# Performance work log

Measured on AMD Instinct MI355X. Metric: run time of the kernel, lower is better.

## Reference

```python
import jax, jax.numpy as jnp
import numpy as np

D_MODEL = 1024
NUM_HEADS = 16
HEAD_DIM = D_MODEL // NUM_HEADS


def setup_inputs() -> dict:
    key = jax.random.key(0)
    ks = jax.random.split(key, 9)
    B, S = 4, 2048
    bound = 1.0 / np.sqrt(D_MODEL)  # nn.Linear default init range
    def lin(kw, kb):
        W = jax.random.uniform(kw, (D_MODEL, D_MODEL), jnp.float32, -bound, bound)
        b = jax.random.uniform(kb, (D_MODEL,), jnp.float32, -bound, bound)
        return W, b
    Wq, bq = lin(ks[0], ks[1])
    Wk, bk = lin(ks[2], ks[3])
    Wv, bv = lin(ks[4], ks[5])
    Wo, bo = lin(ks[6], ks[7])
    x = jax.random.normal(ks[8], (B, S, D_MODEL), jnp.float32)
    return {"x": x, "Wq": Wq, "bq": bq, "Wk": Wk, "bk": bk,
            "Wv": Wv, "bv": bv, "Wo": Wo, "bo": bo}


def reference(x, Wq, bq, Wk, bk, Wv, bv, Wo, bo):
    B, S, _ = x.shape
    scale = 1.0 / np.sqrt(HEAD_DIM)
    # projections; torch Linear is x @ W.T + b; here W stored as [in, out]-style [d,d] already transposed
    def split_heads(t):
        return t.reshape(B, S, NUM_HEADS, HEAD_DIM).transpose(0, 2, 1, 3)  # [B,H,S,Dh]
    q = split_heads(x @ Wq + bq)
    k = split_heads(x @ Wk + bk)
    v = split_heads(x @ Wv + bv)
    scores = jnp.einsum('bhqd,bhkd->bhqk', q, k) * scale  # [B,H,S,S]
    attn = jax.nn.softmax(scores, axis=-1)
    out = jnp.einsum('bhqk,bhkd->bhqd', attn, v)  # [B,H,S,Dh]
    out = out.transpose(0, 2, 1, 3).reshape(B, S, D_MODEL)
    return out @ Wo + bo
```

## Files before the change

kernel.cpp:

```cpp
#include <hip/hip_runtime.h>
#include <hip/hip_bf16.h>

typedef __attribute__((ext_vector_type(8))) short short8;
typedef __attribute__((ext_vector_type(4))) float f32x4;
typedef __attribute__((ext_vector_type(16))) float f32x16;

#define MFMA16(a, b, c) __builtin_amdgcn_mfma_f32_16x16x32_bf16((a), (b), (c), 0, 0, 0)
#define MFMA32(a, b, c) __builtin_amdgcn_mfma_f32_32x32x16_bf16((a), (b), (c), 0, 0, 0)

__device__ __forceinline__ void gload_lds16(const void* g, void* l) {
  __builtin_amdgcn_global_load_lds(
      (const __attribute__((address_space(1))) unsigned int*)g,
      (__attribute__((address_space(3))) unsigned int*)l, 16, 0, 0);
}

__global__ __launch_bounds__(256) void cvt_x(const float* __restrict__ x,
                                             __hip_bfloat16* __restrict__ xb) {
  size_t i = ((size_t)blockIdx.x * 256 + threadIdx.x) * 8;
  float4 a = *(const float4*)(x + i);
  float4 b = *(const float4*)(x + i + 4);
  struct alignas(16) B8 { __hip_bfloat16 h[8]; } o;
  o.h[0] = __float2bfloat16(a.x); o.h[1] = __float2bfloat16(a.y);
  o.h[2] = __float2bfloat16(a.z); o.h[3] = __float2bfloat16(a.w);
  o.h[4] = __float2bfloat16(b.x); o.h[5] = __float2bfloat16(b.y);
  o.h[6] = __float2bfloat16(b.z); o.h[7] = __float2bfloat16(b.w);
  *(B8*)(xb + i) = o;
}

__global__ __launch_bounds__(256) void trans_w(const float* __restrict__ W0,
                                               const float* __restrict__ W1,
                                               const float* __restrict__ W2,
                                               const float* __restrict__ W3,
                                               __hip_bfloat16* __restrict__ Wt) {
  const int which = blockIdx.z;
  const float* W = (which == 0) ? W0 : (which == 1) ? W1 : (which == 2) ? W2 : W3;
  __hip_bfloat16* O = Wt + (size_t)which * 1024 * 1024;
  __shared__ __hip_bfloat16 lds[64][65];
  const int k0 = blockIdx.y * 64, n0 = blockIdx.x * 64;
#pragma unroll
  for (int i = 0; i < 16; ++i) {
    int idx = threadIdx.x + i * 256;
    int r = idx >> 6, c = idx & 63;
    lds[r][c] = __float2bfloat16(W[(size_t)(k0 + r) * 1024 + n0 + c]);
  }
  __syncthreads();
#pragma unroll
  for (int i = 0; i < 16; ++i) {
    int idx = threadIdx.x + i * 256;
    int r = idx >> 6, c = idx & 63;
    O[(size_t)(n0 + r) * 1024 + k0 + c] = lds[c][r];
  }
}

__global__ __launch_bounds__(256) void gemm_qkv(const __hip_bfloat16* __restrict__ A,
                                                const __hip_bfloat16* __restrict__ Wt,
                                                const float* __restrict__ bq,
                                                const float* __restrict__ bk,
                                                const float* __restrict__ bv,
                                                __hip_bfloat16* __restrict__ Qb,
                                                __hip_bfloat16* __restrict__ Kb,
                                                __hip_bfloat16* __restrict__ Vtb) {
  const int K = 1024;
  __shared__ __hip_bfloat16 Asm[128 * 32];
  __shared__ __hip_bfloat16 Bsm[128 * 32];
  const int t = threadIdx.x;
  const int lane = t & 63, w = t >> 6, g = lane >> 4;
  const int bid = (blockIdx.x & 7) * 192 + (blockIdx.x >> 3);
  const int mb0 = (bid / 24) * 128;
  const int nbg = (bid % 24) * 128;
  const int which = nbg >> 10;
  const int nb0 = nbg & 1023;
  const __hip_bfloat16* Bt = Wt + (size_t)which * 1048576;
  const float* bias = (which == 0) ? bq : (which == 1) ? bk : bv;
  const int wr = (w >> 1) * 64, wc = (w & 1) * 64;
  f32x4 acc[4][4] = {};

  for (int k0 = 0; k0 < K; k0 += 32) {
    __syncthreads();
#pragma unroll
    for (int i = 0; i < 2; ++i) {
      int tp = i * 256 + t;
      int row = tp >> 2;
      int slot = (tp & 3) ^ ((row >> 1) & 3);
      gload_lds16(A + (size_t)(mb0 + row) * K + k0 + slot * 8,
                  (char*)Asm + (i * 256 + w * 64) * 16);
    }
#pragma unroll
    for (int i = 0; i < 2; ++i) {
      int tp = i * 256 + t;
      int row = tp >> 2;
      int slot = (tp & 3) ^ ((row >> 1) & 3);
      gload_lds16(Bt + (size_t)(nb0 + row) * K + k0 + slot * 8,
                  (char*)Bsm + (i * 256 + w * 64) * 16);
    }
    asm volatile("s_waitcnt vmcnt(0)" ::: "memory");
    __syncthreads();

    short8 a[4], b[4];
#pragma unroll
    for (int m = 0; m < 4; ++m) {
      int row = wr + m * 16 + (lane & 15);
      a[m] = *(const short8*)((const char*)Asm + row * 64 + ((g ^ ((row >> 1) & 3)) * 16));
    }
#pragma unroll
    for (int n = 0; n < 4; ++n) {
      int row = wc + n * 16 + (lane & 15);
      b[n] = *(const short8*)((const char*)Bsm + row * 64 + ((g ^ ((row >> 1) & 3)) * 16));
    }
#pragma unroll
    for (int m = 0; m < 4; ++m)
#pragma unroll
      for (int n = 0; n < 4; ++n)
        acc[m][n] = MFMA16(a[m], b[n], acc[m][n]);
  }

#pragma unroll
  for (int n = 0; n < 4; ++n) {
    int col = nb0 + wc + n * 16 + (lane & 15);
    float bvv = bias[col];
#pragma unroll
    for (int m = 0; m < 4; ++m) {
#pragma unroll
      for (int r = 0; r < 4; ++r) {
        int row = mb0 + wr + m * 16 + g * 4 + r;
        __hip_bfloat16 hv = __float2bfloat16(acc[m][n][r] + bvv);
        if (which == 2) {
          int bb = row >> 11, s = row & 2047;
          int sp = (s & ~12) | ((s & 4) << 1) | ((s & 8) >> 1);
          Vtb[((size_t)(bb * 1024 + col) << 11) + sp] = hv;
        } else {
          __hip_bfloat16* O = which ? Kb : Qb;
          O[(size_t)row * 1024 + col] = hv;
        }
      }
    }
  }
}

__global__ __launch_bounds__(256) void gemm_o(const __hip_bfloat16* __restrict__ A,
                                              const __hip_bfloat16* __restrict__ Bt,
                                              const float* __restrict__ bias,
                                              float* __restrict__ outp) {
  const int N = 1024, K = 1024;
  __shared__ __hip_bfloat16 Asm[128 * 32];
  __shared__ __hip_bfloat16 Bsm[128 * 32];
  const int t = threadIdx.x;
  const int lane = t & 63, w = t >> 6, g = lane >> 4;
  const int bid = (blockIdx.x & 7) * 64 + (blockIdx.x >> 3);
  const int mb0 = (bid / 8) * 128;
  const int nb0 = (bid % 8) * 128;
  const int wr = (w >> 1) * 64, wc = (w & 1) * 64;
  f32x4 acc[4][4] = {};

  for (int k0 = 0; k0 < K; k0 += 32) {
    __syncthreads();
#pragma unroll
    for (int i = 0; i < 2; ++i) {
      int tp = i * 256 + t;
      int row = tp >> 2;
      int slot = (tp & 3) ^ ((row >> 1) & 3);
      gload_lds16(A + (size_t)(mb0 + row) * K + k0 + slot * 8,
                  (char*)Asm + (i * 256 + w * 64) * 16);
      gload_lds16(Bt + (size_t)(nb0 + row) * K + k0 + slot * 8,
                  (char*)Bsm + (i * 256 + w * 64) * 16);
    }
    asm volatile("s_waitcnt vmcnt(0)" ::: "memory");
    __syncthreads();

    short8 a[4], b[4];
#pragma unroll
    for (int m = 0; m < 4; ++m) {
      int row = wr + m * 16 + (lane & 15);
      a[m] = *(const short8*)((const char*)Asm + row * 64 + ((g ^ ((row >> 1) & 3)) * 16));
    }
#pragma unroll
    for (int n = 0; n < 4; ++n) {
      int row = wc + n * 16 + (lane & 15);
      b[n] = *(const short8*)((const char*)Bsm + row * 64 + ((g ^ ((row >> 1) & 3)) * 16));
    }
#pragma unroll
    for (int m = 0; m < 4; ++m)
#pragma unroll
      for (int n = 0; n < 4; ++n)
        acc[m][n] = MFMA16(a[m], b[n], acc[m][n]);
  }

#pragma unroll
  for (int n = 0; n < 4; ++n) {
    int col = nb0 + wc + n * 16 + (lane & 15);
    float bvv = bias[col];
#pragma unroll
    for (int m = 0; m < 4; ++m)
#pragma unroll
      for (int r = 0; r < 4; ++r) {
        int row = mb0 + wr + m * 16 + g * 4 + r;
        outp[(size_t)row * N + col] = acc[m][n][r] + bvv;
      }
  }
}

__global__ __launch_bounds__(256, 2) void attn_fwd8(const __hip_bfloat16* __restrict__ Q,
                                                    const __hip_bfloat16* __restrict__ Kg,
                                                    const __hip_bfloat16* __restrict__ Vt,
                                                    __hip_bfloat16* __restrict__ ctx) {
  __shared__ __hip_bfloat16 Ksm[2][64 * 64];
  __shared__ __hip_bfloat16 Vsm[2][64 * 64];
  const int t = threadIdx.x, lane = t & 63, w = t >> 6;
  const int l31 = lane & 31, hi = lane >> 5;
  const int bid = (blockIdx.x & 7) * 64 + (blockIdx.x >> 3);
  const int bh = bid >> 3, qt = bid & 7;
  const int b = bh >> 4, h = bh & 15;
  const int qA = qt * 256 + w * 64 + l31;
  const int qB = qA + 32;

  short8 qfA[4], qfB[4];
  {
    const __hip_bfloat16* qp = Q + ((size_t)(b * 2048 + qA)) * 1024 + h * 64 + hi * 8;
#pragma unroll
    for (int c = 0; c < 4; ++c) qfA[c] = *(const short8*)(qp + 16 * c);
    qp += 32 * 1024;
#pragma unroll
    for (int c = 0; c < 4; ++c) qfB[c] = *(const short8*)(qp + 16 * c);
  }
  const __hip_bfloat16* Kbh = Kg + (size_t)b * 2048 * 1024 + h * 64;
  const __hip_bfloat16* Vbh = Vt + (size_t)(b * 16 + h) * 64 * 2048;

  const int srow = t >> 3;
  const int sslot = t & 7;

#define STAGE(buf, ktn)                                                          \
  do {                                                                           \
    _Pragma("unroll") for (int i = 0; i < 2; ++i) {                              \
      int row = i * 32 + srow;                                                   \
      int sl = sslot ^ (row & 7);                                                \
      gload_lds16(Kbh + (size_t)((ktn) + row) * 1024 + sl * 8,                   \
                  (char*)&Ksm[buf][0] + i * 4096 + w * 1024);                    \
      gload_lds16(Vbh + (size_t)row * 2048 + (ktn) + sl * 8,                     \
                  (char*)&Vsm[buf][0] + i * 4096 + w * 1024);                    \
    }                                                                            \
  } while (0)

  f32x16 otA0 = {}, otA1 = {}, otB0 = {}, otB1 = {};
  float lsA0 = 0.f, lsA1 = 0.f, lsB0 = 0.f, lsB1 = 0.f;
  const float CL = 0.18033688011112042f;
  const float NEG = -43.28085122666891f;

  STAGE(0, 0);
  asm volatile("s_waitcnt vmcnt(0)" ::: "memory");
  __syncthreads();

  for (int kt = 0; kt < 2048; kt += 64) {
    const int cur = (kt >> 6) & 1;
    if (kt + 64 < 2048) STAGE(cur ^ 1, kt + 64);

    const char* Kb0 = (const char*)&Ksm[cur][0];
    const char* Vb0 = (const char*)&Vsm[cur][0];

    f32x16 sA0 = {}, sA1 = {}, sB0 = {}, sB1 = {};
    {
      short8 kf[2][4];
#pragma unroll
      for (int s = 0; s < 2; ++s)
#pragma unroll
        for (int c = 0; c < 4; ++c) {
          int row = s * 32 + l31;
          kf[s][c] = *(const short8*)(Kb0 + row * 128 + (((hi + 2 * c) ^ (row & 7)) * 16));
        }
#pragma unroll
      for (int c = 0; c < 4; ++c) {
        sA0 = MFMA32(kf[0][c], qfA[c], sA0);
        sA1 = MFMA32(kf[1][c], qfA[c], sA1);
        sB0 = MFMA32(kf[0][c], qfB[c], sB0);
        sB1 = MFMA32(kf[1][c], qfB[c], sB1);
      }
    }

    short8 vf[2][4];
#pragma unroll
    for (int dt = 0; dt < 2; ++dt)
#pragma unroll
      for (int c = 0; c < 4; ++c) {
        int row = dt * 32 + l31;
        vf[dt][c] = *(const short8*)(Vb0 + row * 128 + (((hi + 2 * c) ^ (row & 7)) * 16));
      }

    {
      unsigned ua[16];
#pragma unroll
      for (int n = 0; n < 8; ++n) {
        float a0 = __builtin_fmaf(sA0[2 * n], CL, NEG);
        float a1 = __builtin_fmaf(sA0[2 * n + 1], CL, NEG);
        float e0, e1;
        asm("v_exp_f32 %0, %1" : "=v"(e0) : "v"(a0));
        asm("v_exp_f32 %0, %1" : "=v"(e1) : "v"(a1));
        lsA0 += e0; lsA1 += e1;
        asm("v_cvt_pk_bf16_f32 %0, %1, %2" : "=v"(ua[n]) : "v"(e0), "v"(e1));
      }
#pragma unroll
      for (int n = 0; n < 8; ++n) {
        float a0 = __builtin_fmaf(sA1[2 * n], CL, NEG);
        float a1 = __builtin_fmaf(sA1[2 * n + 1], CL, NEG);
        float e0, e1;
        asm("v_exp_f32 %0, %1" : "=v"(e0) : "v"(a0));
        asm("v_exp_f32 %0, %1" : "=v"(e1) : "v"(a1));
        lsA0 += e0; lsA1 += e1;
        asm("v_cvt_pk_bf16_f32 %0, %1, %2" : "=v"(ua[8 + n]) : "v"(e0), "v"(e1));
      }
#pragma unroll
      for (int c = 0; c < 4; ++c) {
        union { unsigned u[4]; short8 s8; } pb;
        pb.u[0] = ua[4 * c]; pb.u[1] = ua[4 * c + 1];
        pb.u[2] = ua[4 * c + 2]; pb.u[3] = ua[4 * c + 3];
        otA0 = MFMA32(vf[0][c], pb.s8, otA0);
        otA1 = MFMA32(vf[1][c], pb.s8, otA1);
      }
    }

    {
      unsigned ub[16];
#pragma unroll
      for (int n = 0; n < 8; ++n) {
        float a0 = __builtin_fmaf(sB0[2 * n], CL, NEG);
        float a1 = __builtin_fmaf(sB0[2 * n + 1], CL, NEG);
        float e0, e1;
        asm("v_exp_f32 %0, %1" : "=v"(e0) : "v"(a0));
        asm("v_exp_f32 %0, %1" : "=v"(e1) : "v"(a1));
        lsB0 += e0; lsB1 += e1;
        asm("v_cvt_pk_bf16_f32 %0, %1, %2" : "=v"(ub[n]) : "v"(e0), "v"(e1));
      }
#pragma unroll
      for (int n = 0; n < 8; ++n) {
        float a0 = __builtin_fmaf(sB1[2 * n], CL, NEG);
        float a1 = __builtin_fmaf(sB1[2 * n + 1], CL, NEG);
        float e0, e1;
        asm("v_exp_f32 %0, %1" : "=v"(e0) : "v"(a0));
        asm("v_exp_f32 %0, %1" : "=v"(e1) : "v"(a1));
        lsB0 += e0; lsB1 += e1;
        asm("v_cvt_pk_bf16_f32 %0, %1, %2" : "=v"(ub[8 + n]) : "v"(e0), "v"(e1));
      }
#pragma unroll
      for (int c = 0; c < 4; ++c) {
        union { unsigned u[4]; short8 s8; } pb;
        pb.u[0] = ub[4 * c]; pb.u[1] = ub[4 * c + 1];
        pb.u[2] = ub[4 * c + 2]; pb.u[3] = ub[4 * c + 3];
        otB0 = MFMA32(vf[0][c], pb.s8, otB0);
        otB1 = MFMA32(vf[1][c], pb.s8, otB1);
      }
    }

    asm volatile("s_waitcnt vmcnt(0)" ::: "memory");
    __syncthreads();
  }
#undef STAGE

  float lsumA = lsA0 + lsA1;
  lsumA += __shfl_xor(lsumA, 32);
  float invA = 1.0f / lsumA;
  float lsumB = lsB0 + lsB1;
  lsumB += __shfl_xor(lsumB, 32);
  float invB = 1.0f / lsumB;

  {
    __hip_bfloat16* op = ctx + ((size_t)(b * 2048 + qA)) * 1024 + h * 64 + 4 * hi;
#pragma unroll
    for (int dt = 0; dt < 2; ++dt) {
#pragma unroll
      for (int g = 0; g < 4; ++g) {
        struct alignas(8) H4 { __hip_bfloat16 x[4]; } o4;
#pragma unroll
        for (int e = 0; e < 4; ++e)
          o4.x[e] = __float2bfloat16((dt ? otA1[4 * g + e] : otA0[4 * g + e]) * invA);
        *(H4*)(op + 32 * dt + 8 * g) = o4;
      }
    }
    op += 32 * 1024;
#pragma unroll
    for (int dt = 0; dt < 2; ++dt) {
#pragma unroll
      for (int g = 0; g < 4; ++g) {
        struct alignas(8) H4 { __hip_bfloat16 x[4]; } o4;
#pragma unroll
        for (int e = 0; e < 4; ++e)
          o4.x[e] = __float2bfloat16((dt ? otB1[4 * g + e] : otB0[4 * g + e]) * invB);
        *(H4*)(op + 32 * dt + 8 * g) = o4;
      }
    }
  }
}

extern "C" void kernel_launch(void* const* d_in, const int* in_sizes, int n_in,
                              void* d_out, int out_size, void* d_ws, size_t ws_size,
                              hipStream_t stream) {
  (void)in_sizes; (void)n_in; (void)out_size; (void)ws_size;
  const float* x  = (const float*)d_in[0];
  const float* Wq = (const float*)d_in[1];
  const float* bq = (const float*)d_in[2];
  const float* Wk = (const float*)d_in[3];
  const float* bk = (const float*)d_in[4];
  const float* Wv = (const float*)d_in[5];
  const float* bv = (const float*)d_in[6];
  const float* Wo = (const float*)d_in[7];
  const float* bo = (const float*)d_in[8];
  float* out = (float*)d_out;

  __hip_bfloat16* ws  = (__hip_bfloat16*)d_ws;
  __hip_bfloat16* xb  = ws;
  __hip_bfloat16* Wt  = xb + 8388608;
  __hip_bfloat16* Qb  = Wt + 4194304;
  __hip_bfloat16* Kb  = Qb + 8388608;
  __hip_bfloat16* Vtb = Kb + 8388608;
  __hip_bfloat16* ctx = xb;

  cvt_x<<<4096, 256, 0, stream>>>(x, xb);
  trans_w<<<dim3(16, 16, 4), 256, 0, stream>>>(Wq, Wk, Wv, Wo, Wt);
  gemm_qkv<<<1536, 256, 0, stream>>>(xb, Wt, bq, bk, bv, Qb, Kb, Vtb);
  attn_fwd8<<<512, 256, 0, stream>>>(Qb, Kb, Vtb, ctx);
  gemm_o<<<512, 256, 0, stream>>>(ctx, Wt + 3145728, bo, out);
}
```

Baseline: 217.8 us.

## Switch projection GEMMs to 32x32 MFMA with 64-wide K tiles

Both projection GEMMs (QKV and output) now use the 32x32x16 bf16 MFMA instead of 16x16x32 and double the K tile per LDS stage from 32 to 64. LDS uses an 8-slot XOR swizzle, and launch bounds now request 4 blocks per CU. The aim is fewer barriers and global-to-LDS stages per K sweep and fewer LDS fragment reads per MFMA. In exchange the blocks use twice the LDS, and the epilogue writes now have a different, less contiguous pattern.

```diff
diff --git a/kernel.cpp b/kernel.cpp
--- a/kernel.cpp
+++ b/kernel.cpp
@@ -52,19 +52,19 @@
   }
 }
 
-__global__ __launch_bounds__(256) void gemm_qkv(const __hip_bfloat16* __restrict__ A,
-                                                const __hip_bfloat16* __restrict__ Wt,
-                                                const float* __restrict__ bq,
-                                                const float* __restrict__ bk,
-                                                const float* __restrict__ bv,
-                                                __hip_bfloat16* __restrict__ Qb,
-                                                __hip_bfloat16* __restrict__ Kb,
-                                                __hip_bfloat16* __restrict__ Vtb) {
-  const int K = 1024;
-  __shared__ __hip_bfloat16 Asm[128 * 32];
-  __shared__ __hip_bfloat16 Bsm[128 * 32];
+__global__ __launch_bounds__(256, 4) void gemm_qkv(const __hip_bfloat16* __restrict__ A,
+                                                   const __hip_bfloat16* __restrict__ Wt,
+                                                   const float* __restrict__ bq,
+                                                   const float* __restrict__ bk,
+                                                   const float* __restrict__ bv,
+                                                   __hip_bfloat16* __restrict__ Qb,
+                                                   __hip_bfloat16* __restrict__ Kb,
+                                                   __hip_bfloat16* __restrict__ Vtb) {
+  __shared__ __hip_bfloat16 Asm[128 * 64];
+  __shared__ __hip_bfloat16 Bsm[128 * 64];
   const int t = threadIdx.x;
-  const int lane = t & 63, w = t >> 6, g = lane >> 4;
+  const int lane = t & 63, w = t >> 6;
+  const int l31 = lane & 31, hi = lane >> 5;
   const int bid = (blockIdx.x & 7) * 192 + (blockIdx.x >> 3);
   const int mb0 = (bid / 24) * 128;
   const int nbg = (bid % 24) * 128;
@@ -73,56 +73,54 @@
   const __hip_bfloat16* Bt = Wt + (size_t)which * 1048576;
   const float* bias = (which == 0) ? bq : (which == 1) ? bk : bv;
   const int wr = (w >> 1) * 64, wc = (w & 1) * 64;
-  f32x4 acc[4][4] = {};
-
-  for (int k0 = 0; k0 < K; k0 += 32) {
+  f32x16 acc[2][2] = {};
+
+  for (int k0 = 0; k0 < 1024; k0 += 64) {
     __syncthreads();
 #pragma unroll
-    for (int i = 0; i < 2; ++i) {
+    for (int i = 0; i < 4; ++i) {
       int tp = i * 256 + t;
-      int row = tp >> 2;
-      int slot = (tp & 3) ^ ((row >> 1) & 3);
-      gload_lds16(A + (size_t)(mb0 + row) * K + k0 + slot * 8,
-                  (char*)Asm + (i * 256 + w * 64) * 16);
-    }
-#pragma unroll
-    for (int i = 0; i < 2; ++i) {
+      int row = tp >> 3;
+      int sl = (tp & 7) ^ (row & 7);
+      gload_lds16(A + (size_t)(mb0 + row) * 1024 + k0 + sl * 8, (char*)Asm + tp * 16);
+    }
+#pragma unroll
+    for (int i = 0; i < 4; ++i) {
       int tp = i * 256 + t;
-      int row = tp >> 2;
-      int slot = (tp & 3) ^ ((row >> 1) & 3);
-      gload_lds16(Bt + (size_t)(nb0 + row) * K + k0 + slot * 8,
-                  (char*)Bsm + (i * 256 + w * 64) * 16);
+      int row = tp >> 3;
+      int sl = (tp & 7) ^ (row & 7);
+      gload_lds16(Bt + (size_t)(nb0 + row) * 1024 + k0 + sl * 8, (char*)Bsm + tp * 16);
     }
     asm volatile("s_waitcnt vmcnt(0)" ::: "memory");
     __syncthreads();
 
-    short8 a[4], b[4];
-#pragma unroll
-    for (int m = 0; m < 4; ++m) {
-      int row = wr + m * 16 + (lane & 15);
-      a[m] = *(const short8*)((const char*)Asm + row * 64 + ((g ^ ((row >> 1) & 3)) * 16));
-    }
-#pragma unroll
-    for (int n = 0; n < 4; ++n) {
-      int row = wc + n * 16 + (lane & 15);
-      b[n] = *(const short8*)((const char*)Bsm + row * 64 + ((g ^ ((row >> 1) & 3)) * 16));
-    }
-#pragma unroll
-    for (int m = 0; m < 4; ++m)
-#pragma unroll
-      for (int n = 0; n < 4; ++n)
-        acc[m][n] = MFMA16(a[m], b[n], acc[m][n]);
-  }
-
-#pragma unroll
-  for (int n = 0; n < 4; ++n) {
-    int col = nb0 + wc + n * 16 + (lane & 15);
+#pragma unroll
+    for (int kk = 0; kk < 4; ++kk) {
+      const int sl = ((kk * 2 + hi) ^ (l31 & 7)) * 16;
+      short8 aA[2], bB[2];
+#pragma unroll
+      for (int m = 0; m < 2; ++m)
+        aA[m] = *(const short8*)((const char*)Asm + (wr + m * 32 + l31) * 128 + sl);
+#pragma unroll
+      for (int n = 0; n < 2; ++n)
+        bB[n] = *(const short8*)((const char*)Bsm + (wc + n * 32 + l31) * 128 + sl);
+#pragma unroll
+      for (int m = 0; m < 2; ++m)
+#pragma unroll
+        for (int n = 0; n < 2; ++n)
+          acc[m][n] = MFMA32(aA[m], bB[n], acc[m][n]);
+    }
+  }
+
+#pragma unroll
+  for (int n = 0; n < 2; ++n) {
+    int col = nb0 + wc + n * 32 + l31;
     float bvv = bias[col];
 #pragma unroll
-    for (int m = 0; m < 4; ++m) {
-#pragma unroll
-      for (int r = 0; r < 4; ++r) {
-        int row = mb0 + wr + m * 16 + g * 4 + r;
+    for (int m = 0; m < 2; ++m) {
+#pragma unroll
+      for (int r = 0; r < 16; ++r) {
+        int row = mb0 + wr + m * 32 + (r & 3) + 8 * (r >> 2) + 4 * hi;
         __hip_bfloat16 hv = __float2bfloat16(acc[m][n][r] + bvv);
         if (which == 2) {
           int bb = row >> 11, s = row & 2047;
@@ -137,65 +135,70 @@
   }
 }
 
-__global__ __launch_bounds__(256) void gemm_o(const __hip_bfloat16* __restrict__ A,
-                                              const __hip_bfloat16* __restrict__ Bt,
-                                              const float* __restrict__ bias,
-                                              float* __restrict__ outp) {
-  const int N = 1024, K = 1024;
-  __shared__ __hip_bfloat16 Asm[128 * 32];
-  __shared__ __hip_bfloat16 Bsm[128 * 32];
+__global__ __launch_bounds__(256, 4) void gemm_o(const __hip_bfloat16* __restrict__ A,
+                                                 const __hip_bfloat16* __restrict__ Bt,
+                                                 const float* __restrict__ bias,
+                                                 float* __restrict__ outp) {
+  __shared__ __hip_bfloat16 Asm[128 * 64];
+  __shared__ __hip_bfloat16 Bsm[128 * 64];
   const int t = threadIdx.x;
-  const int lane = t & 63, w = t >> 6, g = lane >> 4;
+  const int lane = t & 63, w = t >> 6;
+  const int l31 = lane & 31, hi = lane >> 5;
   const int bid = (blockIdx.x & 7) * 64 + (blockIdx.x >> 3);
   const int mb0 = (bid / 8) * 128;
   const int nb0 = (bid % 8) * 128;
   const int wr = (w >> 1) * 64, wc = (w & 1) * 64;
-  f32x4 acc[4][4] = {};
-
-  for (int k0 = 0; k0 < K; k0 += 32) {
+  f32x16 acc[2][2] = {};
+
+  for (int k0 = 0; k0 < 1024; k0 += 64) {
     __syncthreads();
 #pragma unroll
-    for (int i = 0; i < 2; ++i) {
+    for (int i = 0; i < 4; ++i) {
       int tp = i * 256 + t;
-      int row = tp >> 2;
-      int slot = (tp & 3) ^ ((row >> 1) & 3);
-      gload_lds16(A + (size_t)(mb0 + row) * K + k0 + slot * 8,
-                  (char*)Asm + (i * 256 + w * 64) * 16);
-      gload_lds16(Bt + (size_t)(nb0 + row) * K + k0 + slot * 8,
-                  (char*)Bsm + (i * 256 + w * 64) * 16);
+      int row = tp >> 3;
+      int sl = (tp & 7) ^ (row & 7);
+      gload_lds16(A + (size_t)(mb0 + row) * 1024 + k0 + sl * 8, (char*)Asm + tp * 16);
+    }
+#pragma unroll
+    for (int i = 0; i < 4; ++i) {
+      int tp = i * 256 + t;
+      int row = tp >> 3;
+      int sl = (tp & 7) ^ (row & 7);
+      gload_lds16(Bt + (size_t)(nb0 + row) * 1024 + k0 + sl * 8, (char*)Bsm + tp * 16);
     }
     asm volatile("s_waitcnt vmcnt(0)" ::: "memory");
     __syncthreads();
 
-    short8 a[4], b[4];
-#pragma unroll
-    for (int m = 0; m < 4; ++m) {
-      int row = wr + m * 16 + (lane & 15);
-      a[m] = *(const short8*)((const char*)Asm + row * 64 + ((g ^ ((row >> 1) & 3)) * 16));
-    }
-#pragma unroll
-    for (int n = 0; n < 4; ++n) {
-      int row = wc + n * 16 + (lane & 15);
-      b[n] = *(const short8*)((const char*)Bsm + row * 64 + ((g ^ ((row >> 1) & 3)) * 16));
-    }
-#pragma unroll
-    for (int m = 0; m < 4; ++m)
-#pragma unroll
-      for (int n = 0; n < 4; ++n)
-        acc[m][n] = MFMA16(a[m], b[n], acc[m][n]);
-  }
-
-#pragma unroll
-  for (int n = 0; n < 4; ++n) {
-    int col = nb0 + wc + n * 16 + (lane & 15);
+#pragma unroll
+    for (int kk = 0; kk < 4; ++kk) {
+      const int sl = ((kk * 2 + hi) ^ (l31 & 7)) * 16;
+      short8 aA[2], bB[2];
+#pragma unroll
+      for (int m = 0; m < 2; ++m)
+        aA[m] = *(const short8*)((const char*)Asm + (wr + m * 32 + l31) * 128 + sl);
+#pragma unroll
+      for (int n = 0; n < 2; ++n)
+        bB[n] = *(const short8*)((const char*)Bsm + (wc + n * 32 + l31) * 128 + sl);
+#pragma unroll
+      for (int m = 0; m < 2; ++m)
+#pragma unroll
+        for (int n = 0; n < 2; ++n)
+          acc[m][n] = MFMA32(aA[m], bB[n], acc[m][n]);
+    }
+  }
+
+#pragma unroll
+  for (int n = 0; n < 2; ++n) {
+    int col = nb0 + wc + n * 32 + l31;
     float bvv = bias[col];
 #pragma unroll
-    for (int m = 0; m < 4; ++m)
-#pragma unroll
-      for (int r = 0; r < 4; ++r) {
-        int row = mb0 + wr + m * 16 + g * 4 + r;
-        outp[(size_t)row * N + col] = acc[m][n][r] + bvv;
-      }
+    for (int m = 0; m < 2; ++m) {
+#pragma unroll
+      for (int r = 0; r < 16; ++r) {
+        int row = mb0 + wr + m * 32 + (r & 3) + 8 * (r >> 2) + 4 * hi;
+        outp[(size_t)row * 1024 + col] = acc[m][n][r] + bvv;
+      }
+    }
   }
 }
 
@@ -211,7 +214,6 @@
   const int bh = bid >> 3, qt = bid & 7;
   const int b = bh >> 4, h = bh & 15;
   const int qA = qt * 256 + w * 64 + l31;
-  const int qB = qA + 32;
 
   short8 qfA[4], qfB[4];
   {
```

New measurement: 219.4 us. No clear change (+0.7%).
